# Kernel tuning notes

Hardware: AMD Instinct MI355X
Metric: run time of the kernel (lower is better)

## Reference

```python
import jax, jax.numpy as jnp
import numpy as np

# ---- model constants (match init_kwargs) ----
NX, NY, H, K, GRID = 32, 1, 64, 3, 5
MID = 2 * H + 1            # 129, middle width of each KAN block
NB = GRID + K              # 8 B-spline basis functions per edge
BATCH = 65536


def _grid_pts():
    # uniform extended grid on [-1, 1] with K extra knots each side: GRID+2K+1 pts
    step = 2.0 / GRID
    return jnp.arange(-K, GRID + K + 1, dtype=jnp.float32) * step - 1.0


def bspline_basis(x):
    """Cox-de Boor B-spline bases. x: [B, I] -> [B, I, GRID+K]."""
    g = _grid_pts()[None, None, :]          # [1,1,P]
    xe = x[..., None]                       # [B,I,1]
    B0 = ((xe >= g[..., :-1]) & (xe < g[..., 1:])).astype(x.dtype)
    Bp = B0
    for p in range(1, K + 1):
        left = (xe - g[..., :-(p + 1)]) / (g[..., p:-1] - g[..., :-(p + 1)])
        right = (g[..., p + 1:] - xe) / (g[..., p + 1:] - g[..., 1:-p])
        Bp = left * Bp[..., :-1] + right * Bp[..., 1:]
    return Bp  # [B, I, NB]


def kan_layer(x, coef, sb, ss, bias):
    """pykan KANLayer: y_o = sum_i sb[i,o]*silu(x_i) + ss[i,o]*spline_io(x_i) + bias_o.
    x: [B,I]; coef: [I,O,NB]; sb, ss: [I,O]; bias: [O]."""
    bs = bspline_basis(x)                                   # [B,I,NB]
    spline = jnp.einsum('bip,iop->bo', bs, coef * ss[:, :, None])
    return jax.nn.silu(x) @ sb + spline + bias


def setup_inputs() -> dict:
    key = jax.random.key(0)
    ks = iter(jax.random.split(key, 40))

    def xavier(k, shape, fan_in, fan_out):
        gain = np.sqrt(2.0)  # relu gain, as in the torch module
        std = gain * np.sqrt(2.0 / (fan_in + fan_out))
        return (std * jax.random.normal(k, shape, dtype=jnp.float32))

    inp = {
        'x': jax.random.normal(next(ks), (BATCH, NX), dtype=jnp.float32),
        'W_in': xavier(next(ks), (NX, H), NX, H),
        'b_in': jnp.zeros((H,), jnp.float32),
        'W_out': xavier(next(ks), (H, NY), H, NY),
    }
    for l in range(2):  # num_hidden_layers KAN blocks, each = 2 KANLayers
        for tag, (din, dout) in [('a', (H, MID)), ('b', (MID, H))]:
            inp[f'coef{l}{tag}'] = xavier(next(ks), (din, dout, NB), din * NB, dout)
            inp[f'sb{l}{tag}'] = xavier(next(ks), (din, dout), din, dout)
            inp[f'ss{l}{tag}'] = jnp.ones((din, dout), jnp.float32)
            inp[f'bias{l}{tag}'] = jnp.zeros((dout,), jnp.float32)
    return inp


def reference(x, W_in, b_in, W_out,
              coef0a, sb0a, ss0a, bias0a, coef0b, sb0b, ss0b, bias0b,
              coef1a, sb1a, ss1a, bias1a, coef1b, sb1b, ss1b, bias1b):
    h = jax.nn.relu(x @ W_in + b_in)
    for (ca, sa, ta, ba, cb, sbb, tb, bb) in (
        (coef0a, sb0a, ss0a, bias0a, coef0b, sb0b, ss0b, bias0b),
        (coef1a, sb1a, ss1a, bias1a, coef1b, sb1b, ss1b, bias1b),
    ):
        h = kan_layer(h, ca, sa, ta, ba)   # H -> 2H+1
        h = kan_layer(h, cb, sbb, tb, bb)  # 2H+1 -> H
    return jax.nn.sigmoid(h @ W_out)       # [B, NY]
```

## Files before the change

### kernel.cpp

```cpp
#include <hip/hip_runtime.h>
#include <math.h>
#include <stdint.h>

#define BATCH 65536
#define TB 64

typedef __fp16   fp16x2 __attribute__((ext_vector_type(2)));
typedef _Float16 half8  __attribute__((ext_vector_type(8)));
typedef float   floatx4 __attribute__((ext_vector_type(4)));

#define SH 68
#define SM 130
#define HM_SLICE (16*SM + 64)

#define WIN 2048
#define KSA 18
#define KSB 39
#define WA (KSA*9*512)
#define WB (KSB*4*512)
#define WTOT (WIN + 2*(WA+WB))

__global__ void setup_weights(
    const float* __restrict__ W_in,
    const float* __restrict__ c0a, const float* __restrict__ sb0a, const float* __restrict__ ss0a,
    const float* __restrict__ c0b, const float* __restrict__ sb0b, const float* __restrict__ ss0b,
    const float* __restrict__ c1a, const float* __restrict__ sb1a, const float* __restrict__ ss1a,
    const float* __restrict__ c1b, const float* __restrict__ sb1b, const float* __restrict__ ss1b,
    _Float16* __restrict__ wt) {
  int idx = blockIdx.x * 256 + threadIdx.x;
  if (idx >= WTOT) return;
  float v = 0.0f;
  if (idx < WIN) {
    int nt = idx >> 9; int r = idx & 511; int l = r >> 3; int j = r & 7;
    int n = nt*16 + (l & 15);
    int k = (l >> 4)*8 + j;
    v = W_in[k*64 + n];
  } else {
    int e2   = idx - WIN;
    int pair = (e2 >= WA + WB) ? 1 : 0;
    int e    = e2 - pair * (WA + WB);
    if (e < WA) {
      const float* coef = pair ? c1a : c0a;
      const float* sb   = pair ? sb1a : sb0a;
      const float* ss   = pair ? ss1a : ss0a;
      int ks = e / 4608; int r = e - ks*4608;
      int nt = r >> 9;   int q = r & 511;
      int l  = q >> 3;   int j = q & 7;
      int n  = nt*16 + (l & 15);
      int k  = ks*32 + (l >> 4)*8 + j;
      if (n < 129) {
        if (k < 512) { int i = k >> 3, p = k & 7; v = ss[i*129+n] * coef[(i*129+n)*8 + p]; }
        else         { int i = k - 512;           v = sb[i*129+n]; }
      }
    } else {
      const float* coef = pair ? c1b : c0b;
      const float* sb   = pair ? sb1b : sb0b;
      const float* ss   = pair ? ss1b : ss0b;
      int eb = e - WA;
      int ks = eb >> 11; int r = eb & 2047;
      int nt = r >> 9;   int q = r & 511;
      int l  = q >> 3;   int j = q & 7;
      int n  = nt*16 + (l & 15);
      int k  = ks*32 + (l >> 4)*8 + j;
      if (k < 1088) { int i = k >> 3, p = k & 7; if (i < 129) v = ss[i*64+n] * coef[(i*64+n)*8 + p]; }
      else          { int i = k - 1088;          if (i < 129) v = sb[i*64+n]; }
    }
  }
  wt[idx] = (_Float16)v;
}

__device__ __forceinline__ half8 feat8(float x) {
  float s  = (x + 2.2f) * 2.5f;
  float mf = floorf(s);
  int   m  = (int)mf;
  float u  = s - mf;
  float t  = 1.0f - u;
  float u2 = u*u;
  float w0 = t*t*t * (1.0f/6.0f);
  float w3 = u2*u * (1.0f/6.0f);
  float w1 = fmaf(u2, fmaf(0.5f, u, -1.0f), 2.0f/3.0f);
  float w2 = 1.0f - w0 - w1 - w3;
  union { fp16x2 h2[2]; uint64_t u64; } P;
  P.h2[0] = __builtin_amdgcn_cvt_pkrtz(w0, w1);
  P.h2[1] = __builtin_amdgcn_cvt_pkrtz(w2, w3);
  uint64_t w01 = (m >= 0 && m <= 10) ? P.u64 : 0ull;
  int sh = (m - 3) * 16;
  uint64_t q0 = (sh >= 0) ? ((sh < 64) ? (w01 << sh) : 0ull) : (w01 >> (-sh));
  uint64_t q1 = (sh >= 64) ? (w01 << (sh - 64))
                           : ((sh > 0) ? (w01 >> (64 - sh)) : 0ull);
  union { uint64_t q[2]; half8 h; } R;
  R.q[0] = q0; R.q[1] = q1;
  return R.h;
}

template<int KSPL, int KSIL, int NT, int SIN, int O, int SOUT>
__device__ __forceinline__ void kan_layer(
    const _Float16* __restrict__ hinw, _Float16* __restrict__ houtw,
    const _Float16* __restrict__ wt, const float* __restrict__ bias, int lane) {
  const int ln = lane & 15;
  const int kq = lane >> 4;
  const half8* __restrict__ bp = (const half8*)wt + lane;
  floatx4 acc[NT];
  #pragma unroll
  for (int j = 0; j < NT; ++j) acc[j] = (floatx4){0.f, 0.f, 0.f, 0.f};

  #pragma unroll 2
  for (int ks = 0; ks < KSPL; ++ks) {
    if ((ks & 7) == 0) __syncthreads();
    float xv = (float)hinw[ln*SIN + ks*4 + kq];
    half8 A = feat8(xv);
    #pragma unroll
    for (int j = 0; j < NT; ++j) {
      half8 B = bp[(ks*NT + j)*64];
      acc[j] = __builtin_amdgcn_mfma_f32_16x16x32_f16(A, B, acc[j], 0, 0, 0);
    }
  }

  __syncthreads();
  #pragma unroll 2
  for (int sk = 0; sk < KSIL; ++sk) {
    half8 h8 = *(const half8*)&hinw[ln*SIN + sk*32 + kq*8];
    union { fp16x2 h2[4]; half8 h8; } A;
    #pragma unroll
    for (int e = 0; e < 4; ++e) {
      float x0 = (float)h8[2*e], x1 = (float)h8[2*e + 1];
      float s0 = x0 / (1.0f + __expf(-x0));
      float s1 = x1 / (1.0f + __expf(-x1));
      A.h2[e] = __builtin_amdgcn_cvt_pkrtz(s0, s1);
    }
    #pragma unroll
    for (int j = 0; j < NT; ++j) {
      half8 B = bp[((KSPL + sk)*NT + j)*64];
      acc[j] = __builtin_amdgcn_mfma_f32_16x16x32_f16(A.h8, B, acc[j], 0, 0, 0);
    }
  }

  #pragma unroll
  for (int j = 0; j < NT; ++j) {
    int col = j*16 + ln;
    if (col < O) {
      float bv = bias[col];
      #pragma unroll
      for (int r = 0; r < 4; ++r)
        houtw[(kq*4 + r)*SOUT + col] = (_Float16)(acc[j][r] + bv);
    }
  }
}

extern "C" __global__ void __launch_bounds__(256, 4)
kan_forward(const float* __restrict__ x, const float* __restrict__ b_in,
            const float* __restrict__ W_out, const _Float16* __restrict__ wt,
            const float* __restrict__ bias0a, const float* __restrict__ bias0b,
            const float* __restrict__ bias1a, const float* __restrict__ bias1b,
            float* __restrict__ out) {
  __shared__ _Float16 hM[4][HM_SLICE];
  __shared__ _Float16 hH[4][16*SH];
  const int t    = threadIdx.x;
  const int wv   = t >> 6;
  const int lane = t & 63;
  const int ln   = lane & 15;
  const int kq   = lane >> 4;
  _Float16* hMw = hM[wv];
  _Float16* hHw = hH[wv];
  const int rbase = blockIdx.x * TB + wv * 16;

  hMw[16*SM + lane] = (_Float16)0.0f;
  if (lane < 16) hMw[lane*SM + 129] = (_Float16)0.0f;

  {
    const float* xr = &x[(rbase + ln)*32 + kq*8];
    float4 v0 = *(const float4*)&xr[0];
    float4 v1 = *(const float4*)&xr[4];
    union { fp16x2 h2[4]; half8 h8; } A;
    A.h2[0] = __builtin_amdgcn_cvt_pkrtz(v0.x, v0.y);
    A.h2[1] = __builtin_amdgcn_cvt_pkrtz(v0.z, v0.w);
    A.h2[2] = __builtin_amdgcn_cvt_pkrtz(v1.x, v1.y);
    A.h2[3] = __builtin_amdgcn_cvt_pkrtz(v1.z, v1.w);
    const half8* bp = (const half8*)wt + lane;
    #pragma unroll
    for (int nt = 0; nt < 4; ++nt) {
      floatx4 z = (floatx4){0.f, 0.f, 0.f, 0.f};
      half8 B = bp[nt*64];
      floatx4 a = __builtin_amdgcn_mfma_f32_16x16x32_f16(A.h8, B, z, 0, 0, 0);
      int col = nt*16 + ln;
      float bv = b_in[col];
      #pragma unroll
      for (int r = 0; r < 4; ++r)
        hHw[(kq*4 + r)*SH + col] = (_Float16)fmaxf(a[r] + bv, 0.0f);
    }
  }

  kan_layer<16,2,9,SH,129,SM>(hHw, hMw, wt + WIN,             bias0a, lane);
  kan_layer<34,5,4,SM, 64,SH>(hMw, hHw, wt + WIN + WA,        bias0b, lane);
  kan_layer<16,2,9,SH,129,SM>(hHw, hMw, wt + WIN + WA + WB,   bias1a, lane);
  kan_layer<34,5,4,SM, 64,SH>(hMw, hHw, wt + WIN + 2*WA + WB, bias1b, lane);

  {
    float s = 0.0f;
    #pragma unroll
    for (int j = 0; j < 16; ++j)
      s = fmaf((float)hHw[ln*SH + kq*16 + j], W_out[kq*16 + j], s);
    s += __shfl_down(s, 32);
    s += __shfl_down(s, 16);
    if (lane < 16) out[rbase + ln] = 1.0f / (1.0f + __expf(-s));
  }
}

extern "C" void kernel_launch(void* const* d_in, const int* in_sizes, int n_in,
                              void* d_out, int out_size, void* d_ws, size_t ws_size,
                              hipStream_t stream) {
  const float* x     = (const float*)d_in[0];
  const float* W_in  = (const float*)d_in[1];
  const float* b_in  = (const float*)d_in[2];
  const float* W_out = (const float*)d_in[3];
  const float* c0a = (const float*)d_in[4];  const float* sb0a = (const float*)d_in[5];
  const float* ss0a= (const float*)d_in[6];  const float* bias0a=(const float*)d_in[7];
  const float* c0b = (const float*)d_in[8];  const float* sb0b = (const float*)d_in[9];
  const float* ss0b= (const float*)d_in[10]; const float* bias0b=(const float*)d_in[11];
  const float* c1a = (const float*)d_in[12]; const float* sb1a = (const float*)d_in[13];
  const float* ss1a= (const float*)d_in[14]; const float* bias1a=(const float*)d_in[15];
  const float* c1b = (const float*)d_in[16]; const float* sb1b = (const float*)d_in[17];
  const float* ss1b= (const float*)d_in[18]; const float* bias1b=(const float*)d_in[19];
  float*    out = (float*)d_out;
  _Float16* wt  = (_Float16*)d_ws;

  setup_weights<<<(WTOT + 255)/256, 256, 0, stream>>>(
      W_in, c0a, sb0a, ss0a, c0b, sb0b, ss0b,
      c1a, sb1a, ss1a, c1b, sb1b, ss1b, wt);

  kan_forward<<<BATCH/TB, 256, 0, stream>>>(
      x, b_in, W_out, wt, bias0a, bias0b, bias1a, bias1b, out);
}
```

Baseline: 188.0 us.

## Merge spline and SiLU K-loops with register prefetch of weight tiles

Merges the spline-basis and SiLU K-loops of each KAN layer into one loop with a runtime branch. Software-prefetches the first few weight B-fragments for the next K-step into registers, so global/L2 latency overlaps the current MFMAs. Also removes the periodic __syncthreads calls inside the K loop, which is safe because each wave owns its own LDS slice. The extra prefetch registers and the branch in the loop may raise register pressure under the 4-blocks-per-CU launch bound.

```diff
diff --git a/kernel.cpp b/kernel.cpp
--- a/kernel.cpp
+++ b/kernel.cpp
@@ -97,6 +97,8 @@
 __device__ __forceinline__ void kan_layer(
     const _Float16* __restrict__ hinw, _Float16* __restrict__ houtw,
     const _Float16* __restrict__ wt, const float* __restrict__ bias, int lane) {
+  constexpr int KTOT = KSPL + KSIL;
+  constexpr int PF   = (NT > 4) ? 4 : NT;
   const int ln = lane & 15;
   const int kq = lane >> 4;
   const half8* __restrict__ bp = (const half8*)wt + lane;
@@ -104,34 +106,42 @@
   #pragma unroll
   for (int j = 0; j < NT; ++j) acc[j] = (floatx4){0.f, 0.f, 0.f, 0.f};
 
+  half8 Bpre[PF];
+  #pragma unroll
+  for (int j = 0; j < PF; ++j) Bpre[j] = bp[j*64];
+
   #pragma unroll 2
-  for (int ks = 0; ks < KSPL; ++ks) {
-    if ((ks & 7) == 0) __syncthreads();
-    float xv = (float)hinw[ln*SIN + ks*4 + kq];
-    half8 A = feat8(xv);
-    #pragma unroll
-    for (int j = 0; j < NT; ++j) {
+  for (int ks = 0; ks < KTOT; ++ks) {
+    half8 A;
+    if (ks < KSPL) {
+      float xv = (float)hinw[ln*SIN + ks*4 + kq];
+      A = feat8(xv);
+    } else {
+      int sk = ks - KSPL;
+      half8 h8 = *(const half8*)&hinw[ln*SIN + sk*32 + kq*8];
+      union { fp16x2 h2[4]; half8 v; } Au;
+      #pragma unroll
+      for (int e = 0; e < 4; ++e) {
+        float x0 = (float)h8[2*e], x1 = (float)h8[2*e + 1];
+        float s0 = x0 / (1.0f + __expf(-x0));
+        float s1 = x1 / (1.0f + __expf(-x1));
+        Au.h2[e] = __builtin_amdgcn_cvt_pkrtz(s0, s1);
+      }
+      A = Au.v;
+    }
+    half8 Bcur[PF];
+    #pragma unroll
+    for (int j = 0; j < PF; ++j) Bcur[j] = Bpre[j];
+    const int nks = (ks + 1 < KTOT) ? (ks + 1) : ks;
+    #pragma unroll
+    for (int j = 0; j < PF; ++j) Bpre[j] = bp[(nks*NT + j)*64];
+    #pragma unroll
+    for (int j = 0; j < PF; ++j)
+      acc[j] = __builtin_amdgcn_mfma_f32_16x16x32_f16(A, Bcur[j], acc[j], 0, 0, 0);
+    #pragma unroll
+    for (int j = PF; j < NT; ++j) {
       half8 B = bp[(ks*NT + j)*64];
       acc[j] = __builtin_amdgcn_mfma_f32_16x16x32_f16(A, B, acc[j], 0, 0, 0);
-    }
-  }
-
-  __syncthreads();
-  #pragma unroll 2
-  for (int sk = 0; sk < KSIL; ++sk) {
-    half8 h8 = *(const half8*)&hinw[ln*SIN + sk*32 + kq*8];
-    union { fp16x2 h2[4]; half8 h8; } A;
-    #pragma unroll
-    for (int e = 0; e < 4; ++e) {
-      float x0 = (float)h8[2*e], x1 = (float)h8[2*e + 1];
-      float s0 = x0 / (1.0f + __expf(-x0));
-      float s1 = x1 / (1.0f + __expf(-x1));
-      A.h2[e] = __builtin_amdgcn_cvt_pkrtz(s0, s1);
-    }
-    #pragma unroll
-    for (int j = 0; j < NT; ++j) {
-      half8 B = bp[((KSPL + sk)*NT + j)*64];
-      acc[j] = __builtin_amdgcn_mfma_f32_16x16x32_f16(A.h8, B, acc[j], 0, 0, 0);
     }
   }
 
```

Measured after the change: 176.7 us. -6.0%, faster.
